# Performance work log

Hardware: AMD Instinct MI355X
Metric: run time of the kernel (lower is better)

## Reference

```python
import jax, jax.numpy as jnp
import numpy as np

B, S, D = 2, 2048, 1024
H, KVH, HD = 16, 4, 64
WINDOW = 64
N_REP = H // KVH
ROPE_THETA = 10000.0


def _rope(x, cos, sin):
    # x: (b, s, h, hd); treat last dim as interleaved (real, imag) pairs
    xr = x.reshape(*x.shape[:-1], HD // 2, 2)
    a, b = xr[..., 0], xr[..., 1]
    c = cos[None, :, None, :]  # (1, s, 1, hd/2)
    s_ = sin[None, :, None, :]
    out = jnp.stack([a * c - b * s_, a * s_ + b * c], axis=-1)
    return out.reshape(x.shape)


def setup_inputs() -> dict:
    key = jax.random.key(0)
    ks = jax.random.split(key, 5)
    x = jax.random.normal(ks[0], (B, S, D), dtype=jnp.float32)
    # rope frequencies (deterministic, as in Mistral/LLaMA)
    inv_freq = 1.0 / (ROPE_THETA ** (np.arange(0, HD, 2, dtype=np.float32) / HD))
    t = np.arange(S, dtype=np.float32)
    freqs = np.outer(t, inv_freq)  # (S, HD/2)
    freqs_cos = jnp.asarray(np.cos(freqs), dtype=jnp.float32)
    freqs_sin = jnp.asarray(np.sin(freqs), dtype=jnp.float32)
    sc = 0.02
    wq = jax.random.normal(ks[1], (D, H * HD), dtype=jnp.float32) * sc
    wk = jax.random.normal(ks[2], (D, KVH * HD), dtype=jnp.float32) * sc
    wv = jax.random.normal(ks[3], (D, KVH * HD), dtype=jnp.float32) * sc
    wo = jax.random.normal(ks[4], (H * HD, D), dtype=jnp.float32) * sc
    return {"x": x, "freqs_cos": freqs_cos, "freqs_sin": freqs_sin,
            "wq": wq, "wk": wk, "wv": wv, "wo": wo}


def reference(x, freqs_cos, freqs_sin, wq, wk, wv, wo):
    b, s, _ = x.shape
    q = (x @ wq).reshape(b, s, H, HD)
    k = (x @ wk).reshape(b, s, KVH, HD)
    v = (x @ wv).reshape(b, s, KVH, HD)
    q = _rope(q, freqs_cos, freqs_sin)
    k = _rope(k, freqs_cos, freqs_sin)
    # repeat_kv (GQA): expand kv heads by n_rep, kv-head-major ordering
    k = jnp.repeat(k, N_REP, axis=2)  # (b, s, H, hd)
    v = jnp.repeat(v, N_REP, axis=2)
    scores = jnp.einsum('bihd,bjhd->bhij', q, k) / jnp.sqrt(jnp.float32(HD))
    pos = jnp.arange(s)
    dist = pos[None, :] - pos[:, None]  # dist[i,j] = j - i
    banned = (dist > 0) | (dist < -WINDOW)  # causal + sliding window of 64
    mask = jnp.where(banned, jnp.float32(-jnp.inf), jnp.float32(0.0))
    scores = scores + mask[None, None, :, :]
    scores = jnp.maximum(scores, -1e9)  # clamp(min=-1e9)
    attn = jax.nn.softmax(scores.astype(jnp.float32), axis=-1).astype(q.dtype)
    out = jnp.einsum('bhij,bjhd->bihd', attn, v).reshape(b, s, H * HD)
    return out @ wo
```

## Files before the change

kernel.cpp:

```cpp
#include <hip/hip_runtime.h>
#include <hip/hip_bf16.h>

constexpr int B = 2, S = 2048, D = 1024;
constexpr int H = 16, KVH = 4, HD = 64;
constexpr int BS = B * S;
constexpr int QS = 1536;

typedef __attribute__((ext_vector_type(8))) short short8;
typedef __attribute__((ext_vector_type(4))) float floatx4;

#define GPTR(p) ((__attribute__((address_space(1))) void*)(p))
#define LPTR(p) ((__attribute__((address_space(3))) void*)(p))

static __device__ __forceinline__ unsigned short f2bf(float f) {
  union { float f; unsigned u; } c{f};
  unsigned r = (c.u + 0x7FFFu + ((c.u >> 16) & 1u)) >> 16;
  return (unsigned short)r;
}

__global__ __launch_bounds__(256) void prep_kernel(
    const float* __restrict__ x,
    const float* __restrict__ wq, const float* __restrict__ wk,
    const float* __restrict__ wv, const float* __restrict__ wo,
    unsigned short* __restrict__ xb,
    unsigned short* __restrict__ wqkvT, unsigned short* __restrict__ woT) {
  int bz = blockIdx.x;
  if (bz < 4096) {
    int t = bz * 256 + threadIdx.x;
    float4 v = ((const float4*)x)[t];
    ushort4 o;
    o.x = f2bf(v.x); o.y = f2bf(v.y); o.z = f2bf(v.z); o.w = f2bf(v.w);
    ((ushort4*)xb)[t] = o;
    return;
  }
  __shared__ float t[32][33];
  int z = bz - 4096;
  int zx = z % 80, zy = z / 80;
  const float* src; unsigned short* dst; int N, dstOff, nb;
  if (zx < 32)      { src = wq; dst = wqkvT; N = 1024; dstOff = 0;    nb = zx; }
  else if (zx < 40) { src = wk; dst = wqkvT; N = 256;  dstOff = 1024; nb = zx - 32; }
  else if (zx < 48) { src = wv; dst = wqkvT; N = 256;  dstOff = 1280; nb = zx - 40; }
  else              { src = wo; dst = woT;   N = 1024; dstOff = 0;    nb = zx - 48; }
  int n0 = nb * 32, k0 = zy * 32;
  int tx = threadIdx.x & 31, ty = threadIdx.x >> 5;
#pragma unroll
  for (int r = 0; r < 4; ++r)
    t[ty + r * 8][tx] = src[(size_t)(k0 + ty + r * 8) * N + n0 + tx];
  __syncthreads();
#pragma unroll
  for (int r = 0; r < 4; ++r)
    dst[(size_t)(dstOff + n0 + ty + r * 8) * D + k0 + tx] = f2bf(t[tx][ty + r * 8]);
}

#define GEMM_PROLOGUE(Aptr, Btptr)                                            \
  __shared__ unsigned short As[4 * 128 * 32];                                 \
  __shared__ unsigned short Bs[4 * 64 * 32];                                  \
  const int tid = threadIdx.x;                                                \
  const int lane = tid & 63, wvid = tid >> 6;                                 \
  const int wy = wvid >> 1, wx = wvid & 1;                                    \
  const int quad = lane >> 4, lrow = lane & 15;                               \
  const size_t row0 = (size_t)blockIdx.x * 128;                               \
  const size_t col0 = (size_t)blockIdx.y * 64;                                \
  floatx4 acc[4][2];                                                          \
  _Pragma("unroll") for (int i = 0; i < 4; ++i)                               \
    _Pragma("unroll") for (int j = 0; j < 2; ++j)                             \
      acc[i][j] = floatx4{0.f, 0.f, 0.f, 0.f};                                \
  const int arow = wvid * 32 + (lane >> 2);                                   \
  const int brow = wvid * 16 + (lane >> 2);                                   \
  const int schk = (lane & 3) * 8;                                            \
  const unsigned short* gA = (Aptr) + (row0 + arow) * 1024 + schk;            \
  const unsigned short* gB = (Btptr) + (col0 + brow) * 1024 + schk;           \
  char* ldsA = (char*)As + wvid * 2048;                                       \
  char* ldsB = (char*)Bs + wvid * 1024;                                       \
  for (int k0 = 0; k0 < 1024; k0 += 128) {                                    \
    __syncthreads();                                                          \
    _Pragma("unroll") for (int hf = 0; hf < 4; ++hf) {                        \
      __builtin_amdgcn_global_load_lds(GPTR(gA + k0 + hf * 32),               \
                                       LPTR(ldsA + hf * 8192), 16, 0, 0);     \
      __builtin_amdgcn_global_load_lds(GPTR(gA + 16 * 1024 + k0 + hf * 32),   \
                                       LPTR(ldsA + hf * 8192 + 1024), 16, 0, 0); \
      __builtin_amdgcn_global_load_lds(GPTR(gB + k0 + hf * 32),               \
                                       LPTR(ldsB + hf * 4096), 16, 0, 0);     \
    }                                                                         \
    __syncthreads();                                                          \
    _Pragma("unroll") for (int hf = 0; hf < 4; ++hf) {                        \
      short8 af[4], bg[2];                                                    \
      _Pragma("unroll") for (int mi = 0; mi < 4; ++mi)                        \
        af[mi] = *(const short8*)&As[hf * 4096 +                              \
                                     (wy * 64 + mi * 16 + lrow) * 32 + quad * 8]; \
      _Pragma("unroll") for (int ni = 0; ni < 2; ++ni)                        \
        bg[ni] = *(const short8*)&Bs[hf * 2048 +                              \
                                     (wx * 32 + ni * 16 + lrow) * 32 + quad * 8]; \
      _Pragma("unroll") for (int mi = 0; mi < 4; ++mi)                        \
        _Pragma("unroll") for (int ni = 0; ni < 2; ++ni)                      \
          acc[mi][ni] = __builtin_amdgcn_mfma_f32_16x16x32_bf16(              \
              af[mi], bg[ni], acc[mi][ni], 0, 0, 0);                          \
    }                                                                         \
  }

__global__ __launch_bounds__(256) void gemm_qkv_kernel(
    const unsigned short* __restrict__ A, const unsigned short* __restrict__ Bt,
    const float* __restrict__ cs, const float* __restrict__ sn,
    unsigned short* __restrict__ qb, unsigned short* __restrict__ kb,
    unsigned short* __restrict__ vt) {
  GEMM_PROLOGUE(A, Bt)

  const int col_wave = (int)col0 + wx * 32;
  const int h = col_wave >> 6;
  const int hc = col_wave & 63;
  const int sb = (int)(row0 & 2047) + wy * 64;
  const int bidx = (int)(row0 >> 11);

  if (h < 20) {
    unsigned short* dst = (h < 16) ? qb : kb;
    const int dstride = (h < 16) ? 1024 : 256;
    const int dcol = (h < 16) ? col_wave : (col_wave - 1024);
    const bool ev = (lrow & 1) == 0;
#pragma unroll
    for (int mi = 0; mi < 4; ++mi) {
#pragma unroll
      for (int ni = 0; ni < 2; ++ni) {
        int ff = (hc + ni * 16 + lrow) >> 1;
#pragma unroll
        for (int r = 0; r < 4; ++r) {
          int s = sb + mi * 16 + quad * 4 + r;
          float v = acc[mi][ni][r];
          float p = __shfl_xor(v, 1);
          float c = cs[s * 32 + ff];
          float si = sn[s * 32 + ff];
          float o = ev ? (v * c - p * si) : (v * c + p * si);
          size_t row = row0 + wy * 64 + mi * 16 + quad * 4 + r;
          dst[row * dstride + dcol + ni * 16 + lrow] = f2bf(o);
        }
      }
    }
  } else {
    const int kvh = h - 20;
    const int g = bidx * KVH + kvh;
#pragma unroll
    for (int mi = 0; mi < 4; ++mi) {
#pragma unroll
      for (int ni = 0; ni < 2; ++ni) {
        int d = hc + ni * 16 + lrow;
        int s0 = sb + mi * 16 + quad * 4;
        ushort4 o;
        o.x = f2bf(acc[mi][ni][0]); o.y = f2bf(acc[mi][ni][1]);
        o.z = f2bf(acc[mi][ni][2]); o.w = f2bf(acc[mi][ni][3]);
        *(ushort4*)&vt[((size_t)(g * 64 + d)) * S + s0] = o;
      }
    }
  }
}

__global__ __launch_bounds__(256) void gemm_bt_kernel(
    const unsigned short* __restrict__ A, const unsigned short* __restrict__ Bt,
    float* __restrict__ C, int N) {
  GEMM_PROLOGUE(A, Bt)

#pragma unroll
  for (int mi = 0; mi < 4; ++mi)
#pragma unroll
    for (int ni = 0; ni < 2; ++ni) {
      size_t col = col0 + wx * 32 + ni * 16 + lrow;
      size_t rowb = row0 + wy * 64 + mi * 16 + quad * 4;
#pragma unroll
      for (int r = 0; r < 4; ++r)
        C[(rowb + r) * N + col] = acc[mi][ni][r];
    }
}

__global__ __launch_bounds__(256) void attn_kernel(
    const unsigned short* __restrict__ qb,
    const unsigned short* __restrict__ kb,
    const unsigned short* __restrict__ vt,
    unsigned short* __restrict__ ao) {
  __shared__ __align__(16) unsigned short plds[4][16][104];
  const int w = threadIdx.x >> 6, lane = threadIdx.x & 63;
  const int lrow = lane & 15, quad = lane >> 4;
  const int wg = blockIdx.x * 4 + w;
  const int h = wg & (H - 1);
  const int qblk = wg >> 4;
  const int i0 = (qblk & (S / 16 - 1)) * 16;
  const int b = qblk >> 7;
  const int kvh = h >> 2;
  const int jbase = i0 - 80;

  const unsigned short* qrow = qb + (size_t)(b * S + i0 + lrow) * 1024 + h * 64 + quad * 8;
  short8 qf0 = *(const short8*)qrow;
  short8 qf1 = *(const short8*)(qrow + 32);

  floatx4 sc[6];
#pragma unroll
  for (int t = 0; t < 6; ++t) {
    int j = jbase + t * 16 + lrow;
    int jc = j < 0 ? 0 : j;
    const unsigned short* krow = kb + (size_t)(b * S + jc) * 256 + kvh * 64 + quad * 8;
    short8 kf0 = *(const short8*)krow;
    short8 kf1 = *(const short8*)(krow + 32);
    floatx4 a = {0.f, 0.f, 0.f, 0.f};
    a = __builtin_amdgcn_mfma_f32_16x16x32_bf16(qf0, kf0, a, 0, 0, 0);
    a = __builtin_amdgcn_mfma_f32_16x16x32_bf16(qf1, kf1, a, 0, 0, 0);
    sc[t] = a;
  }

  float sv[6][4];
  float mx[4] = {-1e30f, -1e30f, -1e30f, -1e30f};
#pragma unroll
  for (int t = 0; t < 6; ++t) {
    int j = jbase + t * 16 + lrow;
#pragma unroll
    for (int r = 0; r < 4; ++r) {
      int dji = (i0 + quad * 4 + r) - j;
      bool valid = (j >= 0) && (dji >= 0) && (dji <= 64);
      float s = valid ? sc[t][r] * 0.125f : -1e30f;
      sv[t][r] = s;
      mx[r] = fmaxf(mx[r], s);
    }
  }
#pragma unroll
  for (int r = 0; r < 4; ++r)
#pragma unroll
    for (int off = 8; off > 0; off >>= 1)
      mx[r] = fmaxf(mx[r], __shfl_xor(mx[r], off));

  float ls[4] = {0.f, 0.f, 0.f, 0.f};
#pragma unroll
  for (int t = 0; t < 6; ++t)
#pragma unroll
    for (int r = 0; r < 4; ++r) {
      float e = __expf(sv[t][r] - mx[r]);
      sv[t][r] = e;
      ls[r] += e;
    }
#pragma unroll
  for (int r = 0; r < 4; ++r) {
#pragma unroll
    for (int off = 8; off > 0; off >>= 1)
      ls[r] += __shfl_xor(ls[r], off);
    ls[r] = 1.f / ls[r];
  }
#pragma unroll
  for (int t = 0; t < 6; ++t)
#pragma unroll
    for (int r = 0; r < 4; ++r)
      plds[w][quad * 4 + r][t * 16 + lrow] = f2bf(sv[t][r] * ls[r]);
  __syncthreads();

  floatx4 oc[4];
#pragma unroll
  for (int mt = 0; mt < 4; ++mt) oc[mt] = floatx4{0.f, 0.f, 0.f, 0.f};
  const unsigned short* vbase = vt + (size_t)(b * KVH + kvh) * 64 * S;
#pragma unroll
  for (int c = 0; c < 3; ++c) {
    short8 pf = *(const short8*)&plds[w][lrow][c * 32 + quad * 8];
    int j = jbase + c * 32 + quad * 8;
    int jc = j < 0 ? 0 : j;
#pragma unroll
    for (int mt = 0; mt < 4; ++mt) {
      short8 vf = *(const short8*)(vbase + (size_t)(mt * 16 + lrow) * S + jc);
      oc[mt] = __builtin_amdgcn_mfma_f32_16x16x32_bf16(vf, pf, oc[mt], 0, 0, 0);
    }
  }

#pragma unroll
  for (int mt = 0; mt < 4; ++mt) {
    ushort4 o;
    o.x = f2bf(oc[mt][0]); o.y = f2bf(oc[mt][1]);
    o.z = f2bf(oc[mt][2]); o.w = f2bf(oc[mt][3]);
    *(ushort4*)(ao + (size_t)(b * S + i0 + lrow) * 1024 + h * 64 + mt * 16 + quad * 4) = o;
  }
}

extern "C" void kernel_launch(void* const* d_in, const int* in_sizes, int n_in,
                              void* d_out, int out_size, void* d_ws, size_t ws_size,
                              hipStream_t stream) {
  const float* x  = (const float*)d_in[0];
  const float* fc = (const float*)d_in[1];
  const float* fs = (const float*)d_in[2];
  const float* wq = (const float*)d_in[3];
  const float* wk = (const float*)d_in[4];
  const float* wv = (const float*)d_in[5];
  const float* wo = (const float*)d_in[6];
  float* out = (float*)d_out;

  char* base = (char*)d_ws;
  unsigned short* xb    = (unsigned short*)base;
  unsigned short* wqkvT = (unsigned short*)(base + (8u << 20));
  unsigned short* woT   = (unsigned short*)(base + (11u << 20));
  unsigned short* qb    = (unsigned short*)(base + (13u << 20));
  unsigned short* kb    = (unsigned short*)(base + (21u << 20));
  unsigned short* vT    = (unsigned short*)(base + (23u << 20));
  unsigned short* ao    = (unsigned short*)(base + (25u << 20));

  prep_kernel<<<4096 + 2560, 256, 0, stream>>>(x, wq, wk, wv, wo, xb, wqkvT, woT);

  gemm_qkv_kernel<<<dim3(BS / 128, QS / 64), 256, 0, stream>>>(
      xb, wqkvT, fc, fs, qb, kb, vT);

  attn_kernel<<<(BS / 16) * H / 4, 256, 0, stream>>>(qb, kb, vT, ao);

  gemm_bt_kernel<<<dim3(BS / 128, D / 64), 256, 0, stream>>>(ao, woT, out, D);
}
```

Before: 139.7 us.

## Group attention block by KV head and stage K/V tiles in LDS

Remaps attention blocks so the four warps in a block share one KV head (the four query heads of a GQA group) over the same query tile. The block cooperatively loads the 96-row K window and the V^T slice into padded shared memory once, and each warp reads its K and V fragments from LDS. This removes four-fold redundant global K/V loads per block. In exchange it adds LDS use and a barrier. Attention is only part of the total pipeline, which also includes the GEMMs.

```diff
diff --git a/kernel.cpp b/kernel.cpp
--- a/kernel.cpp
+++ b/kernel.cpp
@@ -174,29 +174,50 @@
     const unsigned short* __restrict__ kb,
     const unsigned short* __restrict__ vt,
     unsigned short* __restrict__ ao) {
+  __shared__ __align__(16) unsigned short Ks[96 * 72];
+  __shared__ __align__(16) unsigned short Vs[64 * 104];
   __shared__ __align__(16) unsigned short plds[4][16][104];
-  const int w = threadIdx.x >> 6, lane = threadIdx.x & 63;
+  const int tid = threadIdx.x;
+  const int w = tid >> 6, lane = tid & 63;
   const int lrow = lane & 15, quad = lane >> 4;
-  const int wg = blockIdx.x * 4 + w;
-  const int h = wg & (H - 1);
-  const int qblk = wg >> 4;
+  const int kvh = blockIdx.x & 3;
+  const int qblk = blockIdx.x >> 2;
+  const int h = kvh * 4 + w;
   const int i0 = (qblk & (S / 16 - 1)) * 16;
   const int b = qblk >> 7;
-  const int kvh = h >> 2;
   const int jbase = i0 - 80;
-
-  const unsigned short* qrow = qb + (size_t)(b * S + i0 + lrow) * 1024 + h * 64 + quad * 8;
+  const int bS = b * S;
+
+#pragma unroll
+  for (int it = 0; it < 3; ++it) {
+    int c = tid + it * 256;
+    int rr = c >> 3, oo = (c & 7) * 8;
+    int j = jbase + rr;
+    j = j < 0 ? 0 : j;
+    *(uint4*)&Ks[rr * 72 + oo] =
+        *(const uint4*)&kb[(size_t)(bS + j) * 256 + kvh * 64 + oo];
+  }
+  const unsigned short* vbase = vt + (size_t)(b * KVH + kvh) * 64 * S;
+#pragma unroll
+  for (int it = 0; it < 3; ++it) {
+    int c = tid + it * 256;
+    int rr = c / 12, oo = c % 12;
+    int j = jbase + oo * 8;
+    j = j < 0 ? 0 : j;
+    *(uint4*)&Vs[rr * 104 + oo * 8] = *(const uint4*)&vbase[(size_t)rr * S + j];
+  }
+  __syncthreads();
+
+  const unsigned short* qrow = qb + (size_t)(bS + i0 + lrow) * 1024 + h * 64 + quad * 8;
   short8 qf0 = *(const short8*)qrow;
   short8 qf1 = *(const short8*)(qrow + 32);
 
   floatx4 sc[6];
 #pragma unroll
   for (int t = 0; t < 6; ++t) {
-    int j = jbase + t * 16 + lrow;
-    int jc = j < 0 ? 0 : j;
-    const unsigned short* krow = kb + (size_t)(b * S + jc) * 256 + kvh * 64 + quad * 8;
-    short8 kf0 = *(const short8*)krow;
-    short8 kf1 = *(const short8*)(krow + 32);
+    int kr = t * 16 + lrow;
+    short8 kf0 = *(const short8*)&Ks[kr * 72 + quad * 8];
+    short8 kf1 = *(const short8*)&Ks[kr * 72 + 32 + quad * 8];
     floatx4 a = {0.f, 0.f, 0.f, 0.f};
     a = __builtin_amdgcn_mfma_f32_16x16x32_bf16(qf0, kf0, a, 0, 0, 0);
     a = __builtin_amdgcn_mfma_f32_16x16x32_bf16(qf1, kf1, a, 0, 0, 0);
@@ -249,15 +270,12 @@
   floatx4 oc[4];
 #pragma unroll
   for (int mt = 0; mt < 4; ++mt) oc[mt] = floatx4{0.f, 0.f, 0.f, 0.f};
-  const unsigned short* vbase = vt + (size_t)(b * KVH + kvh) * 64 * S;
 #pragma unroll
   for (int c = 0; c < 3; ++c) {
     short8 pf = *(const short8*)&plds[w][lrow][c * 32 + quad * 8];
-    int j = jbase + c * 32 + quad * 8;
-    int jc = j < 0 ? 0 : j;
 #pragma unroll
     for (int mt = 0; mt < 4; ++mt) {
-      short8 vf = *(const short8*)(vbase + (size_t)(mt * 16 + lrow) * S + jc);
+      short8 vf = *(const short8*)&Vs[(mt * 16 + lrow) * 104 + c * 32 + quad * 8];
       oc[mt] = __builtin_amdgcn_mfma_f32_16x16x32_bf16(vf, pf, oc[mt], 0, 0, 0);
     }
   }
@@ -267,7 +285,7 @@
     ushort4 o;
     o.x = f2bf(oc[mt][0]); o.y = f2bf(oc[mt][1]);
     o.z = f2bf(oc[mt][2]); o.w = f2bf(oc[mt][3]);
-    *(ushort4*)(ao + (size_t)(b * S + i0 + lrow) * 1024 + h * 64 + mt * 16 + quad * 4) = o;
+    *(ushort4*)(ao + (size_t)(bS + i0 + lrow) * 1024 + h * 64 + mt * 16 + quad * 4) = o;
   }
 }
 
```

Measured after the change: 133.6 us, median of 2. -4.3%, faster.
